# Optimization experiments

Hardware: AMD Instinct MI355X
Metric: run time of the kernel (lower is better)

The kernel has to match this reference:

```python
import math
import jax, jax.numpy as jnp
import numpy as np

NUM_HEADS = 32
NUM_KV_HEADS = 8
HEAD_SIZE = 128
FEATURE_DIM = 64
SEQ_LEN = 2048
WINDOW_SIZE = 64
EPS = 1e-12
MASK_VALUE = -100000000.0


def _make_masks(n: int, w: int):
    # block-diagonal ones(w,w) tiles, plus the rolled (sub-diagonal) tiles
    m = math.ceil(n / w)
    mask = np.kron(np.eye(m), np.ones((w, w)))
    mask = mask + np.roll(mask, -w, axis=-1)
    mask = mask[:n, :n]
    mask_window = np.tril(mask).astype(bool)[None, None]          # [1,1,n,n]
    mask_linear = np.tril(1.0 - mask).astype(bool)[None, None]    # [1,1,n,n]
    return jnp.asarray(mask_window), jnp.asarray(mask_linear)


def _feature_map(w, x):
    # f(x) = clamp(cat(softmax(xW), softmax(-xW)), min=eps)
    z = jnp.einsum('hdf,bhld->bhlf', w, x)
    return jnp.clip(
        jnp.concatenate([jax.nn.softmax(z, axis=-1), jax.nn.softmax(-z, axis=-1)], axis=-1),
        EPS, None)


def setup_inputs() -> dict:
    key = jax.random.key(0)
    ks = jax.random.split(key, 6)
    return {
        'query': jax.random.normal(ks[0], (SEQ_LEN, NUM_HEADS * HEAD_SIZE), dtype=jnp.float32),
        'key': jax.random.normal(ks[1], (SEQ_LEN, NUM_KV_HEADS * HEAD_SIZE), dtype=jnp.float32),
        'value': jax.random.normal(ks[2], (SEQ_LEN, NUM_KV_HEADS * HEAD_SIZE), dtype=jnp.float32),
        'fmap_q_w': 0.02 * jax.random.normal(ks[3], (NUM_HEADS, HEAD_SIZE, FEATURE_DIM), dtype=jnp.float32),
        'fmap_k_w': 0.02 * jax.random.normal(ks[4], (NUM_HEADS, HEAD_SIZE, FEATURE_DIM), dtype=jnp.float32),
        'window_factors': jax.random.normal(ks[5], (1, NUM_HEADS, 1, 1), dtype=jnp.float32),
    }


def reference(query, key, value, fmap_q_w, fmap_k_w, window_factors):
    T = query.shape[0]
    q = query.reshape(T, NUM_HEADS, HEAD_SIZE)
    k = key.reshape(T, NUM_KV_HEADS, HEAD_SIZE)
    v = value.reshape(T, NUM_KV_HEADS, HEAD_SIZE)
    rep = NUM_HEADS // NUM_KV_HEADS
    k = jnp.repeat(k, rep, axis=1)
    v = jnp.repeat(v, rep, axis=1)
    # [T,H,D] -> [1,H,T,D]
    q = jnp.moveaxis(q, 0, -2)[None]
    k = jnp.moveaxis(k, 0, -2)[None]
    v = jnp.moveaxis(v, 0, -2)[None]

    f_q = _feature_map(fmap_q_w, q)  # [1,H,T,2F]
    f_k = _feature_map(fmap_k_w, k)
    wf = jax.nn.sigmoid(window_factors)

    mask_window, mask_linear = _make_masks(SEQ_LEN, WINDOW_SIZE)
    mask_window = mask_window[:, :, :T, :T]
    mask_linear = mask_linear[:, :, :T, :T]

    # sliding-window softmax term
    a_sm = jnp.einsum('bhmd,bhnd->bhmn', q, k) * (HEAD_SIZE ** -0.5)
    a_sm = jnp.where(mask_window, a_sm, MASK_VALUE)
    a_sm_max = jnp.max(a_sm, axis=-1, keepdims=True)
    a_sm = wf * jnp.exp(a_sm - a_sm_max)
    sum_sm = jnp.sum(a_sm, axis=-1, keepdims=True)

    # linear feature-map term (linear_factor = 1)
    a_ln = jnp.einsum('bhmd,bhnd->bhmn', f_q, f_k)
    a_ln = jnp.where(mask_linear, a_ln, 0.0)
    sum_ln = jnp.sum(a_ln, axis=-1, keepdims=True)

    y = jnp.einsum('bhmn,bhnd->bhmd', a_sm + a_ln, v)
    return y / (sum_sm + sum_ln)
```

## Files before the change

### kernel.cpp

```cpp
#include <hip/hip_runtime.h>
#include <math.h>

#define T_SEQ 2048
#define NH    32
#define NKV   8
#define HS    128
#define FD    64
#define NBLK  32
#define SCAN_NB 30
#define EPSF  1e-12f
#define LDP   136
#define STP   129

typedef unsigned short u16;
typedef __bf16 bf16x8 __attribute__((ext_vector_type(8)));
typedef float  f32x4  __attribute__((ext_vector_type(4)));

__device__ __forceinline__ u16 f2b(float f) {
  unsigned u = __builtin_bit_cast(unsigned, f);
  return (u16)((u + 0x7fffu + ((u >> 16) & 1u)) >> 16);
}

#define FKT_OFF 0
#define ST_OFF  16777216
#define VT_OFF  54525952
#define WT_OFF  58720256
#define KB_OFF  59768832

__device__ __forceinline__ void stage_bf(u16* buf, const u16* __restrict__ src, int tid) {
#pragma unroll
  for (int i = 0; i < 4; ++i) {
    int idx = tid * 8 + i * 2048, rr = idx >> 7, c = idx & 127;
    *(uint4*)(buf + rr * LDP + c) = *(const uint4*)(src + idx);
  }
}
__device__ __forceinline__ void stage_vt(u16* buf, const u16* __restrict__ vts,
                                         int rofs, int kb0, int B, int tid) {
#pragma unroll
  for (int i = 0; i < 4; ++i) {
    int idx = tid * 8 + i * 2048, rr = idx >> 7, c = idx & 127;
    int key = (c < 64) ? (kb0 * 64 + c) : (B * 64 + (c - 64));
    *(uint4*)(buf + rr * LDP + c) = *(const uint4*)(vts + (size_t)(rr + rofs) * T_SEQ + key);
  }
}

__global__ __launch_bounds__(256) void k_pre(
    const float* __restrict__ wq, const float* __restrict__ wk,
    const float* __restrict__ vg,
    u16* __restrict__ WT, u16* __restrict__ VT)
{
  __shared__ float sB[128 * 68];
  const int bx = blockIdx.x, tid = threadIdx.x;

  if (bx < 64) {
    const int h = bx >> 1, isk = bx & 1;
    const float* src = (isk ? wk : wq) + (size_t)h * HS * FD;
    for (int idx = tid * 4; idx < 8192; idx += 1024) {
      int r = idx >> 6, c = idx & 63;
      *(float4*)(sB + r * 68 + c) = *(const float4*)(src + idx);
    }
    __syncthreads();
    u16* dst = WT + ((size_t)(isk * NH + h)) * 8192;
    for (int i = 0; i < 8; ++i) {
      int ch = tid + i * 256;
      int f = ch >> 5, d4 = (ch & 31) * 4;
      ushort4 u;
      u.x = f2b(sB[(d4 + 0) * 68 + f]);
      u.y = f2b(sB[(d4 + 1) * 68 + f]);
      u.z = f2b(sB[(d4 + 2) * 68 + f]);
      u.w = f2b(sB[(d4 + 3) * 68 + f]);
      *(ushort4*)(dst + f * 128 + d4) = u;
    }
  } else {
    const int idx2 = bx - 64;
    const int b = idx2 & 31, kvh = idx2 >> 5;
    float* sV = sB;
    for (int idx = tid * 4; idx < 8192; idx += 1024) {
      int r = idx >> 7, c = idx & 127;
      *(float4*)(sV + r * 129 + c) = *(const float4*)(vg + (size_t)(b * 64 + r) * (NKV * HS) + kvh * HS + c);
    }
    __syncthreads();
    const int lane = tid & 63, w = tid >> 6;
#pragma unroll
    for (int i = 0; i < 32; ++i) {
      int d = w * 32 + i;
      VT[((size_t)(kvh * 128 + d)) * T_SEQ + b * 64 + lane] = f2b(sV[lane * 129 + d]);
    }
  }
}

__global__ __launch_bounds__(256) void k_fmap(
    const float* __restrict__ kg, const u16* __restrict__ WT,
    u16* __restrict__ FKT, u16* __restrict__ KBB)
{
  __shared__ __align__(16) u16 smem[2 * 64 * 136];
  u16* sX = smem;
  u16* sW = smem + 64 * 136;
  const int lt = blockIdx.x, h = blockIdx.y;
  const int tid = threadIdx.x, lane = tid & 63, w = tid >> 6;
  const int quad = lane >> 4, txn = lane & 15;

  const float* xbase = kg + (h >> 2) * HS;
  const int    xstr  = NKV * HS;
  for (int idx = tid * 4; idx < 8192; idx += 1024) {
    int r = idx >> 7, c = idx & 127;
    float4 v4 = *(const float4*)(xbase + (size_t)(lt * 64 + r) * xstr + c);
    ushort4 u; u.x = f2b(v4.x); u.y = f2b(v4.y); u.z = f2b(v4.z); u.w = f2b(v4.w);
    *(ushort4*)(sX + r * 136 + c) = u;
  }
  const u16* wt = WT + ((size_t)(NH + h)) * 8192;
  for (int i = 0; i < 4; ++i) {
    int ch = tid + i * 256;
    int row = ch >> 4, d8 = (ch & 15) * 8;
    *(uint4*)(sW + row * 136 + d8) = *(const uint4*)(wt + row * 128 + d8);
  }
  __syncthreads();

  if ((h & 3) == 0) {
    u16* ob = KBB + ((size_t)((h >> 2) * NBLK + lt)) * 8192;
    for (int i = 0; i < 4; ++i) {
      int ch = tid + i * 256;
      int row = ch >> 4, d8 = (ch & 15) * 8;
      *(uint4*)(ob + row * 128 + d8) = *(const uint4*)(sX + row * 136 + d8);
    }
  }

  const int arow = w * 16 + txn;
  const f32x4 vzero = {0.f, 0.f, 0.f, 0.f};
  f32x4 zt[4] = {vzero, vzero, vzero, vzero};
#pragma unroll
  for (int ks = 0; ks < 4; ++ks) {
    bf16x8 a = *(const bf16x8*)(sX + arow * 136 + ks * 32 + quad * 8);
#pragma unroll
    for (int nt = 0; nt < 4; ++nt) {
      bf16x8 bb = *(const bf16x8*)(sW + (nt * 16 + txn) * 136 + ks * 32 + quad * 8);
      zt[nt] = __builtin_amdgcn_mfma_f32_16x16x32_bf16(a, bb, zt[nt], 0, 0, 0);
    }
  }

  float E1[4][4], E2[4][4];
#pragma unroll
  for (int r = 0; r < 4; ++r) {
    float zv[4];
    float mx = -1e30f, mn = 1e30f;
#pragma unroll
    for (int nt = 0; nt < 4; ++nt) {
      zv[nt] = zt[nt][r];
      mx = fmaxf(mx, zv[nt]); mn = fminf(mn, zv[nt]);
    }
#pragma unroll
    for (int o = 1; o < 16; o <<= 1) {
      mx = fmaxf(mx, __shfl_xor(mx, o));
      mn = fminf(mn, __shfl_xor(mn, o));
    }
    float e1[4], e2[4], s1 = 0.f, s2 = 0.f;
#pragma unroll
    for (int nt = 0; nt < 4; ++nt) {
      e1[nt] = __expf(zv[nt] - mx); s1 += e1[nt];
      e2[nt] = __expf(mn - zv[nt]); s2 += e2[nt];
    }
#pragma unroll
    for (int o = 1; o < 16; o <<= 1) { s1 += __shfl_xor(s1, o); s2 += __shfl_xor(s2, o); }
    float r1 = 1.f / s1, r2 = 1.f / s2;
#pragma unroll
    for (int nt = 0; nt < 4; ++nt) {
      E1[r][nt] = fmaxf(e1[nt] * r1, EPSF);
      E2[r][nt] = fmaxf(e2[nt] * r2, EPSF);
    }
  }

  __syncthreads();

#pragma unroll
  for (int r = 0; r < 4; ++r) {
    int j = w * 16 + quad * 4 + r;
#pragma unroll
    for (int nt = 0; nt < 4; ++nt) {
      sX[(nt * 16 + txn) * 68 + j]        = f2b(E1[r][nt]);
      sX[(nt * 16 + txn + 64) * 68 + j]   = f2b(E2[r][nt]);
    }
  }
  __syncthreads();
  u16* ob = FKT + (size_t)h * 128 * T_SEQ + lt * 64;
  for (int i = 0; i < 8; ++i) {
    int ch = tid + i * 256;
    int row = ch >> 4, j4 = (ch & 15) * 4;
    *(ushort4*)(ob + (size_t)row * T_SEQ + j4) = *(const ushort4*)(sX + row * 68 + j4);
  }
}

__global__ __launch_bounds__(256) void k_scan(
    const u16* __restrict__ FKT, const u16* __restrict__ VT, u16* __restrict__ ST)
{
  __shared__ __align__(16) u16 sVT[16 * 72];
  __shared__ __align__(16) u16 sFK[64 * 72];
  const int L = blockIdx.x + 8 * blockIdx.y + 16 * blockIdx.z;
  const int xcd = L & 7, j = L >> 3;
  const int hsub = j & 3, fh = (j >> 2) & 1, dc = j >> 3;
  const int h = xcd * 4 + hsub;
  const int tid = threadIdx.x, lane = tid & 63, w = tid >> 6;
  const int quad = lane >> 4, txn = lane & 15;
  const bool doz = (dc == 0);

  bf16x8 vone;
#pragma unroll
  for (int jj = 0; jj < 8; ++jj) vone[jj] = (__bf16)1.0f;

  const u16* vbase = VT + ((size_t)((h >> 2) * 128 + dc * 16)) * T_SEQ;
  const u16* fbase = FKT + ((size_t)(h * 128 + fh * 64)) * T_SEQ;

  const int srow = tid >> 4, sj4 = (tid & 15) * 4;
  ushort4 rv, rf[4];
  rv = *(const ushort4*)(vbase + (size_t)srow * T_SEQ + sj4);
#pragma unroll
  for (int i = 0; i < 4; ++i) {
    int ch = tid + i * 256;
    int fr = ch >> 4, fj4 = (ch & 15) * 4;
    rf[i] = *(const ushort4*)(fbase + (size_t)fr * T_SEQ + fj4);
  }

  const f32x4 vzero = {0.f, 0.f, 0.f, 0.f};
  f32x4 acc = vzero, zacc = vzero;

  for (int b = 0; b < SCAN_NB; ++b) {
    __syncthreads();
    *(ushort4*)(sVT + srow * 72 + sj4) = rv;
#pragma unroll
    for (int i = 0; i < 4; ++i) {
      int ch = tid + i * 256;
      int fr = ch >> 4, fj4 = (ch & 15) * 4;
      *(ushort4*)(sFK + fr * 72 + fj4) = rf[i];
    }
    __syncthreads();
    if (b + 1 < SCAN_NB) {
      rv = *(const ushort4*)(vbase + (size_t)srow * T_SEQ + (b + 1) * 64 + sj4);
#pragma unroll
      for (int i = 0; i < 4; ++i) {
        int ch = tid + i * 256;
        int fr = ch >> 4, fj4 = (ch & 15) * 4;
        rf[i] = *(const ushort4*)(fbase + (size_t)fr * T_SEQ + (b + 1) * 64 + fj4);
      }
    }
#pragma unroll
    for (int ks = 0; ks < 2; ++ks) {
      bf16x8 a  = *(const bf16x8*)(sVT + txn * 72 + ks * 32 + quad * 8);
      bf16x8 bb = *(const bf16x8*)(sFK + (w * 16 + txn) * 72 + ks * 32 + quad * 8);
      acc = __builtin_amdgcn_mfma_f32_16x16x32_bf16(a, bb, acc, 0, 0, 0);
      if (doz) zacc = __builtin_amdgcn_mfma_f32_16x16x32_bf16(vone, bb, zacc, 0, 0, 0);
    }
    u16* Sb = ST + (((size_t)(h * NBLK + b)) * STP + dc * 16) * 128 + fh * 64;
#pragma unroll
    for (int r = 0; r < 4; ++r)
      Sb[(quad * 4 + r) * 128 + w * 16 + txn] = f2b(acc[r]);
    if (doz && quad == 0)
      ST[(((size_t)(h * NBLK + b)) * STP + 128) * 128 + fh * 64 + w * 16 + txn] = f2b(zacc[0]);
  }
}

__global__ __launch_bounds__(256, 4) void k_main(
    const float* __restrict__ qg, const u16* __restrict__ KBB,
    const u16* __restrict__ WT, const u16* __restrict__ ST,
    const u16* __restrict__ VT, const float* __restrict__ wfac,
    float* __restrict__ out)
{
  __shared__ __align__(16) u16 RA[64 * LDP];
  __shared__ __align__(16) u16 RB[64 * LDP];
  __shared__ __align__(16) u16 sz[128];
  const int L = blockIdx.x + 32 * blockIdx.y;
  const int xcd = L & 7, j = L >> 3;
  const int hsub = j & 3, B = j >> 2;
  const int h = xcd * 4 + hsub;
  const int tid = threadIdx.x;
  const int lane = tid & 63, w = tid >> 6;
  const int quad = lane >> 4, txn = lane & 15;
  const int arow = w * 16 + txn;
  const int koff = quad * 8;

  const f32x4 vzero = {0.f, 0.f, 0.f, 0.f};
  f32x4 y[8];
#pragma unroll
  for (int t = 0; t < 8; ++t) y[t] = vzero;
  float sln[4] = {0.f, 0.f, 0.f, 0.f};
  const bf16x8 bzero = {0, 0, 0, 0, 0, 0, 0, 0};

  const int kb0 = (B >= 1) ? B - 1 : 0;
  const u16* ktB   = KBB + ((size_t)((h >> 2) * NBLK + B)) * 8192;
  const u16* ktP   = KBB + ((size_t)((h >> 2) * NBLK + kb0)) * 8192;
  const u16* vts   = VT  + (size_t)((h >> 2) * 128) * T_SEQ;

  for (int idx = tid * 4; idx < 8192; idx += 1024) {
    int r = idx >> 7, c = idx & 127;
    float4 v4 = *(const float4*)(qg + (size_t)(B * 64 + r) * (NH * HS) + h * HS + c);
    ushort4 u; u.x = f2b(v4.x); u.y = f2b(v4.y); u.z = f2b(v4.z); u.w = f2b(v4.w);
    *(ushort4*)(RA + r * LDP + c) = u;
  }
  if (B >= 2) stage_bf(RB, WT + (size_t)h * 8192, tid);
  __syncthreads();

  f32x4 zt[4] = {vzero, vzero, vzero, vzero};
  if (B >= 2) {
#pragma unroll
    for (int ks = 0; ks < 4; ++ks) {
      bf16x8 a = *(const bf16x8*)(RA + arow * LDP + ks * 32 + koff);
#pragma unroll
      for (int nt = 0; nt < 4; ++nt) {
        bf16x8 bb = *(const bf16x8*)(RB + (nt * 16 + txn) * LDP + ks * 32 + koff);
        zt[nt] = __builtin_amdgcn_mfma_f32_16x16x32_bf16(a, bb, zt[nt], 0, 0, 0);
      }
    }
  }
  __syncthreads();
  stage_bf(RB, ktB, tid);

  unsigned Epk[4][4];
  if (B >= 2) {
#pragma unroll
    for (int r = 0; r < 4; ++r) {
      float zv[4];
      float mx = -1e30f, mn = 1e30f;
#pragma unroll
      for (int nt = 0; nt < 4; ++nt) {
        zv[nt] = zt[nt][r];
        mx = fmaxf(mx, zv[nt]); mn = fminf(mn, zv[nt]);
      }
#pragma unroll
      for (int o = 1; o < 16; o <<= 1) {
        mx = fmaxf(mx, __shfl_xor(mx, o));
        mn = fminf(mn, __shfl_xor(mn, o));
      }
      float e1[4], e2[4], s1 = 0.f, s2 = 0.f;
#pragma unroll
      for (int nt = 0; nt < 4; ++nt) {
        e1[nt] = __expf(zv[nt] - mx); s1 += e1[nt];
        e2[nt] = __expf(mn - zv[nt]); s2 += e2[nt];
      }
#pragma unroll
      for (int o = 1; o < 16; o <<= 1) { s1 += __shfl_xor(s1, o); s2 += __shfl_xor(s2, o); }
      float r1 = 1.f / s1, r2 = 1.f / s2;
#pragma unroll
      for (int nt = 0; nt < 4; ++nt) {
        unsigned lo = f2b(fmaxf(e1[nt] * r1, EPSF));
        unsigned hi = f2b(fmaxf(e2[nt] * r2, EPSF));
        Epk[r][nt] = lo | (hi << 16);
      }
    }
  }
  __syncthreads();

  f32x4 s[8];
#pragma unroll
  for (int t = 0; t < 8; ++t) s[t] = vzero;
#pragma unroll
  for (int ks = 0; ks < 4; ++ks) {
    bf16x8 a = *(const bf16x8*)(RA + arow * LDP + ks * 32 + koff);
#pragma unroll
    for (int t = 0; t < 4; ++t) {
      bf16x8 bb = *(const bf16x8*)(RB + (t * 16 + txn) * LDP + ks * 32 + koff);
      s[4 + t] = __builtin_amdgcn_mfma_f32_16x16x32_bf16(a, bb, s[4 + t], 0, 0, 0);
    }
  }

  if (B >= 1) {
    __syncthreads();
    stage_bf(RB, ktP, tid);
    __syncthreads();
#pragma unroll
    for (int ks = 0; ks < 4; ++ks) {
      bf16x8 a = *(const bf16x8*)(RA + arow * LDP + ks * 32 + koff);
#pragma unroll
      for (int t = 0; t < 4; ++t) {
        bf16x8 bb = *(const bf16x8*)(RB + (t * 16 + txn) * LDP + ks * 32 + koff);
        s[t] = __builtin_amdgcn_mfma_f32_16x16x32_bf16(a, bb, s[t], 0, 0, 0);
      }
    }
  }

  float wf = wfac[h];
  wf = 1.f / (1.f + __expf(-wf));
  const float scale = 0.08838834764831845f;
  float ssum[4];
#pragma unroll
  for (int r = 0; r < 4; ++r) {
    const int irow = w * 16 + quad * 4 + r;
    float sv[8];
    float m = -1e30f;
#pragma unroll
    for (int t = 0; t < 8; ++t) {
      float x = s[t][r] * scale;
      bool msk = (t < 4) ? (B == 0) : ((t - 4) * 16 + txn > irow);
      x = msk ? -1e30f : x;
      sv[t] = x;
      m = fmaxf(m, x);
    }
#pragma unroll
    for (int o = 1; o < 16; o <<= 1) m = fmaxf(m, __shfl_xor(m, o));
    float ss = 0.f;
#pragma unroll
    for (int t = 0; t < 8; ++t) {
      float e = (sv[t] > -1e29f) ? wf * __expf(sv[t] - m) : 0.f;
      ss += e;
      RA[irow * LDP + t * 16 + txn] = f2b(e);
    }
#pragma unroll
    for (int o = 1; o < 16; o <<= 1) ss += __shfl_xor(ss, o);
    ssum[r] = ss;
  }
  __syncthreads();

  stage_vt(RB, vts, 0, kb0, B, tid);
  __syncthreads();
#pragma unroll
  for (int ks = 0; ks < 4; ++ks) {
    if (B == 0 && ks < 2) continue;
    bf16x8 a = *(const bf16x8*)(RA + arow * LDP + ks * 32 + koff);
#pragma unroll
    for (int t = 0; t < 4; ++t) {
      bf16x8 bb = *(const bf16x8*)(RB + (t * 16 + txn) * LDP + ks * 32 + koff);
      y[t] = __builtin_amdgcn_mfma_f32_16x16x32_bf16(a, bb, y[t], 0, 0, 0);
    }
  }
  __syncthreads();

  stage_vt(RB, vts, 64, kb0, B, tid);
  __syncthreads();
#pragma unroll
  for (int ks = 0; ks < 4; ++ks) {
    if (B == 0 && ks < 2) continue;
    bf16x8 a = *(const bf16x8*)(RA + arow * LDP + ks * 32 + koff);
#pragma unroll
    for (int t = 4; t < 8; ++t) {
      bf16x8 bb = *(const bf16x8*)(RB + (t * 16 + txn - 64) * LDP + ks * 32 + koff);
      y[t] = __builtin_amdgcn_mfma_f32_16x16x32_bf16(a, bb, y[t], 0, 0, 0);
    }
  }

  if (B >= 2) {
    __syncthreads();
#pragma unroll
    for (int r = 0; r < 4; ++r) {
      int row = w * 16 + quad * 4 + r;
#pragma unroll
      for (int nt = 0; nt < 4; ++nt) {
        RA[row * LDP + nt * 16 + txn]      = (u16)(Epk[r][nt] & 0xffffu);
        RA[row * LDP + 64 + nt * 16 + txn] = (u16)(Epk[r][nt] >> 16);
      }
    }
    const u16* ssrc = ST + ((size_t)(h * NBLK + (B - 2))) * (STP * 128);
    stage_bf(RB, ssrc, tid);
    if (tid < 32) *(ushort4*)(sz + tid * 4) = *(const ushort4*)(ssrc + 16384 + tid * 4);
    __syncthreads();
    f32x4 yz = vzero;
#pragma unroll
    for (int ks = 0; ks < 4; ++ks) {
      bf16x8 a = *(const bf16x8*)(RA + arow * LDP + ks * 32 + koff);
#pragma unroll
      for (int t = 0; t < 4; ++t) {
        bf16x8 bb = *(const bf16x8*)(RB + (t * 16 + txn) * LDP + ks * 32 + koff);
        y[t] = __builtin_amdgcn_mfma_f32_16x16x32_bf16(a, bb, y[t], 0, 0, 0);
      }
      bf16x8 bz = (txn == 0) ? *(const bf16x8*)(sz + ks * 32 + koff) : bzero;
      yz = __builtin_amdgcn_mfma_f32_16x16x32_bf16(a, bz, yz, 0, 0, 0);
    }
    __syncthreads();
    stage_bf(RB, ssrc + 8192, tid);
    __syncthreads();
#pragma unroll
    for (int ks = 0; ks < 4; ++ks) {
      bf16x8 a = *(const bf16x8*)(RA + arow * LDP + ks * 32 + koff);
#pragma unroll
      for (int t = 4; t < 8; ++t) {
        bf16x8 bb = *(const bf16x8*)(RB + (t * 16 + txn - 64) * LDP + ks * 32 + koff);
        y[t] = __builtin_amdgcn_mfma_f32_16x16x32_bf16(a, bb, y[t], 0, 0, 0);
      }
    }
#pragma unroll
    for (int r = 0; r < 4; ++r) sln[r] = __shfl(yz[r], lane & 48);
  }

  const size_t obase = ((size_t)h * T_SEQ + B * 64) * HS;
#pragma unroll
  for (int r = 0; r < 4; ++r) {
    float inv = 1.f / (ssum[r] + sln[r]);
    int irow = w * 16 + quad * 4 + r;
#pragma unroll
    for (int t = 0; t < 8; ++t)
      out[obase + (size_t)irow * HS + t * 16 + txn] = y[t][r] * inv;
  }
}

extern "C" void kernel_launch(void* const* d_in, const int* in_sizes, int n_in,
                              void* d_out, int out_size, void* d_ws, size_t ws_size,
                              hipStream_t stream) {
  const float* q    = (const float*)d_in[0];
  const float* k    = (const float*)d_in[1];
  const float* v    = (const float*)d_in[2];
  const float* wq   = (const float*)d_in[3];
  const float* wk   = (const float*)d_in[4];
  const float* wfac = (const float*)d_in[5];
  float* out = (float*)d_out;
  char* wsb = (char*)d_ws;

  u16* FKT = (u16*)(wsb + FKT_OFF);
  u16* ST  = (u16*)(wsb + ST_OFF);
  u16* VT  = (u16*)(wsb + VT_OFF);
  u16* WT  = (u16*)(wsb + WT_OFF);
  u16* KBB = (u16*)(wsb + KB_OFF);

  k_pre  <<<dim3(320),      256, 0, stream>>>(wq, wk, v, WT, VT);
  k_fmap <<<dim3(NBLK, NH), 256, 0, stream>>>(k, WT, FKT, KBB);
  k_scan <<<dim3(8, 2, NH), 256, 0, stream>>>(FKT, VT, ST);
  k_main <<<dim3(NBLK, NH), 256, 0, stream>>>(q, KBB, WT, ST, VT, wfac, out);
}
```

Baseline: 161.5 us.

## Split k_main key and output columns across two wave groups with 512 threads

The main attention kernel moves from 256 to 512 threads per block. The new waves split the key columns of the score tile and the output columns of the PV and state products, with each wave group doing half the MFMA work. Row max and row sums are now combined across the two wave halves through a small shared-memory buffer with extra barriers. Staging is reorganised into half-tiles so each group works from the right rows. The aim is more waves in flight to hide latency, at the cost of extra synchronisation and redundant feature-map projection work in both halves.

```diff
diff --git a/kernel.cpp b/kernel.cpp
--- a/kernel.cpp
+++ b/kernel.cpp
@@ -26,23 +26,6 @@
 #define VT_OFF  54525952
 #define WT_OFF  58720256
 #define KB_OFF  59768832
-
-__device__ __forceinline__ void stage_bf(u16* buf, const u16* __restrict__ src, int tid) {
-#pragma unroll
-  for (int i = 0; i < 4; ++i) {
-    int idx = tid * 8 + i * 2048, rr = idx >> 7, c = idx & 127;
-    *(uint4*)(buf + rr * LDP + c) = *(const uint4*)(src + idx);
-  }
-}
-__device__ __forceinline__ void stage_vt(u16* buf, const u16* __restrict__ vts,
-                                         int rofs, int kb0, int B, int tid) {
-#pragma unroll
-  for (int i = 0; i < 4; ++i) {
-    int idx = tid * 8 + i * 2048, rr = idx >> 7, c = idx & 127;
-    int key = (c < 64) ? (kb0 * 64 + c) : (B * 64 + (c - 64));
-    *(uint4*)(buf + rr * LDP + c) = *(const uint4*)(vts + (size_t)(rr + rofs) * T_SEQ + key);
-  }
-}
 
 __global__ __launch_bounds__(256) void k_pre(
     const float* __restrict__ wq, const float* __restrict__ wk,
@@ -257,7 +240,7 @@
   }
 }
 
-__global__ __launch_bounds__(256, 4) void k_main(
+__global__ __launch_bounds__(512, 6) void k_main(
     const float* __restrict__ qg, const u16* __restrict__ KBB,
     const u16* __restrict__ WT, const u16* __restrict__ ST,
     const u16* __restrict__ VT, const float* __restrict__ wfac,
@@ -266,35 +249,75 @@
   __shared__ __align__(16) u16 RA[64 * LDP];
   __shared__ __align__(16) u16 RB[64 * LDP];
   __shared__ __align__(16) u16 sz[128];
+  __shared__ float sred[256];
   const int L = blockIdx.x + 32 * blockIdx.y;
-  const int xcd = L & 7, j = L >> 3;
-  const int hsub = j & 3, B = j >> 2;
+  const int xcd = L & 7, jj = L >> 3;
+  const int hsub = jj & 3, B = jj >> 2;
   const int h = xcd * 4 + hsub;
   const int tid = threadIdx.x;
   const int lane = tid & 63, w = tid >> 6;
+  const int wq_ = w & 3, wt = w >> 2;
   const int quad = lane >> 4, txn = lane & 15;
-  const int arow = w * 16 + txn;
+  const int arow = wq_ * 16 + txn;
   const int koff = quad * 8;
 
   const f32x4 vzero = {0.f, 0.f, 0.f, 0.f};
-  f32x4 y[8];
-#pragma unroll
-  for (int t = 0; t < 8; ++t) y[t] = vzero;
+  f32x4 y[4];
+#pragma unroll
+  for (int t = 0; t < 4; ++t) y[t] = vzero;
   float sln[4] = {0.f, 0.f, 0.f, 0.f};
   const bf16x8 bzero = {0, 0, 0, 0, 0, 0, 0, 0};
 
   const int kb0 = (B >= 1) ? B - 1 : 0;
-  const u16* ktB   = KBB + ((size_t)((h >> 2) * NBLK + B)) * 8192;
-  const u16* ktP   = KBB + ((size_t)((h >> 2) * NBLK + kb0)) * 8192;
-  const u16* vts   = VT  + (size_t)((h >> 2) * 128) * T_SEQ;
-
-  for (int idx = tid * 4; idx < 8192; idx += 1024) {
+  const u16* ktB = KBB + ((size_t)((h >> 2) * NBLK + B)) * 8192;
+  const u16* ktP = KBB + ((size_t)((h >> 2) * NBLK + kb0)) * 8192;
+  const u16* vts = VT  + (size_t)((h >> 2) * 128) * T_SEQ;
+  const u16* wqt = WT  + (size_t)h * 8192;
+  const u16* ssrc = ST + ((size_t)(h * NBLK + (B >= 2 ? B - 2 : 0))) * (STP * 128);
+
+  auto stage_full = [&](const u16* __restrict__ src) {
+#pragma unroll
+    for (int i = 0; i < 2; ++i) {
+      int idx = tid * 8 + i * 4096, rr = idx >> 7, c = idx & 127;
+      *(uint4*)(RB + rr * LDP + c) = *(const uint4*)(src + idx);
+    }
+  };
+  auto stage_qk = [&](int p) {
+#pragma unroll
+    for (int i = 0; i < 2; ++i) {
+      int idx = tid * 8 + i * 4096, rr = idx >> 7, c = idx & 127;
+      const u16* src = (rr < 32) ? (ktB + (p * 32 + rr) * 128)
+                                 : (ktP + (p * 32 + rr - 32) * 128);
+      *(uint4*)(RB + rr * LDP + c) = *(const uint4*)(src + c);
+    }
+  };
+  auto stage_v = [&](int p) {
+#pragma unroll
+    for (int i = 0; i < 2; ++i) {
+      int idx = tid * 8 + i * 4096, rr = idx >> 7, c = idx & 127;
+      int d = (rr < 32) ? (p * 32 + rr) : (64 + p * 32 + rr - 32);
+      int key = (c < 64) ? (kb0 * 64 + c) : (B * 64 + (c - 64));
+      *(uint4*)(RB + rr * LDP + c) = *(const uint4*)(vts + (size_t)d * T_SEQ + key);
+    }
+  };
+  auto stage_s = [&](int p) {
+#pragma unroll
+    for (int i = 0; i < 2; ++i) {
+      int idx = tid * 8 + i * 4096, rr = idx >> 7, c = idx & 127;
+      int d = (rr < 32) ? (p * 32 + rr) : (64 + p * 32 + rr - 32);
+      *(uint4*)(RB + rr * LDP + c) = *(const uint4*)(ssrc + d * 128 + c);
+    }
+  };
+
+#pragma unroll
+  for (int i = 0; i < 4; ++i) {
+    int idx = tid * 4 + i * 2048;
     int r = idx >> 7, c = idx & 127;
     float4 v4 = *(const float4*)(qg + (size_t)(B * 64 + r) * (NH * HS) + h * HS + c);
     ushort4 u; u.x = f2b(v4.x); u.y = f2b(v4.y); u.z = f2b(v4.z); u.w = f2b(v4.w);
     *(ushort4*)(RA + r * LDP + c) = u;
   }
-  if (B >= 2) stage_bf(RB, WT + (size_t)h * 8192, tid);
+  if (B >= 2) stage_full(wqt);
   __syncthreads();
 
   f32x4 zt[4] = {vzero, vzero, vzero, vzero};
@@ -310,7 +333,7 @@
     }
   }
   __syncthreads();
-  stage_bf(RB, ktB, tid);
+  stage_qk(0);
 
   unsigned Epk[4][4];
   if (B >= 2) {
@@ -347,130 +370,156 @@
   }
   __syncthreads();
 
-  f32x4 s[8];
-#pragma unroll
-  for (int t = 0; t < 8; ++t) s[t] = vzero;
+  f32x4 s[4];
+#pragma unroll
+  for (int t = 0; t < 4; ++t) s[t] = vzero;
 #pragma unroll
   for (int ks = 0; ks < 4; ++ks) {
     bf16x8 a = *(const bf16x8*)(RA + arow * LDP + ks * 32 + koff);
 #pragma unroll
-    for (int t = 0; t < 4; ++t) {
-      bf16x8 bb = *(const bf16x8*)(RB + (t * 16 + txn) * LDP + ks * 32 + koff);
-      s[4 + t] = __builtin_amdgcn_mfma_f32_16x16x32_bf16(a, bb, s[4 + t], 0, 0, 0);
-    }
-  }
-
-  if (B >= 1) {
-    __syncthreads();
-    stage_bf(RB, ktP, tid);
-    __syncthreads();
-#pragma unroll
-    for (int ks = 0; ks < 4; ++ks) {
-      bf16x8 a = *(const bf16x8*)(RA + arow * LDP + ks * 32 + koff);
-#pragma unroll
-      for (int t = 0; t < 4; ++t) {
-        bf16x8 bb = *(const bf16x8*)(RB + (t * 16 + txn) * LDP + ks * 32 + koff);
-        s[t] = __builtin_amdgcn_mfma_f32_16x16x32_bf16(a, bb, s[t], 0, 0, 0);
-      }
+    for (int tl = 0; tl < 2; ++tl) {
+      if (wt == 0 && B == 0) continue;
+      int row = (wt ? 0 : 32) + tl * 16 + txn;
+      bf16x8 bb = *(const bf16x8*)(RB + row * LDP + ks * 32 + koff);
+      s[tl] = __builtin_amdgcn_mfma_f32_16x16x32_bf16(a, bb, s[tl], 0, 0, 0);
+    }
+  }
+  __syncthreads();
+  stage_qk(1);
+  __syncthreads();
+#pragma unroll
+  for (int ks = 0; ks < 4; ++ks) {
+    bf16x8 a = *(const bf16x8*)(RA + arow * LDP + ks * 32 + koff);
+#pragma unroll
+    for (int tl = 0; tl < 2; ++tl) {
+      if (wt == 0 && B == 0) continue;
+      int row = (wt ? 0 : 32) + tl * 16 + txn;
+      bf16x8 bb = *(const bf16x8*)(RB + row * LDP + ks * 32 + koff);
+      s[2 + tl] = __builtin_amdgcn_mfma_f32_16x16x32_bf16(a, bb, s[2 + tl], 0, 0, 0);
     }
   }
 
   float wf = wfac[h];
   wf = 1.f / (1.f + __expf(-wf));
   const float scale = 0.08838834764831845f;
+  float mh[4];
+#pragma unroll
+  for (int r = 0; r < 4; ++r) {
+    const int irow = wq_ * 16 + quad * 4 + r;
+    float m = -1e30f;
+#pragma unroll
+    for (int sl = 0; sl < 4; ++sl) {
+      float x = s[sl][r] * scale;
+      bool msk = wt ? (sl * 16 + txn > irow) : (B == 0);
+      x = msk ? -1e30f : x;
+      s[sl][r] = x;
+      m = fmaxf(m, x);
+    }
+#pragma unroll
+    for (int o = 1; o < 16; o <<= 1) m = fmaxf(m, __shfl_xor(m, o));
+    mh[r] = m;
+  }
+  if (txn == 0) {
+#pragma unroll
+    for (int r = 0; r < 4; ++r) sred[wt * 64 + wq_ * 16 + quad * 4 + r] = mh[r];
+  }
+  __syncthreads();
+
   float ssum[4];
 #pragma unroll
   for (int r = 0; r < 4; ++r) {
-    const int irow = w * 16 + quad * 4 + r;
-    float sv[8];
-    float m = -1e30f;
-#pragma unroll
-    for (int t = 0; t < 8; ++t) {
-      float x = s[t][r] * scale;
-      bool msk = (t < 4) ? (B == 0) : ((t - 4) * 16 + txn > irow);
-      x = msk ? -1e30f : x;
-      sv[t] = x;
-      m = fmaxf(m, x);
-    }
-#pragma unroll
-    for (int o = 1; o < 16; o <<= 1) m = fmaxf(m, __shfl_xor(m, o));
+    const int irow = wq_ * 16 + quad * 4 + r;
+    float m = fmaxf(mh[r], sred[(wt ^ 1) * 64 + wq_ * 16 + quad * 4 + r]);
     float ss = 0.f;
 #pragma unroll
-    for (int t = 0; t < 8; ++t) {
-      float e = (sv[t] > -1e29f) ? wf * __expf(sv[t] - m) : 0.f;
+    for (int sl = 0; sl < 4; ++sl) {
+      float e = (s[sl][r] > -1e29f) ? wf * __expf(s[sl][r] - m) : 0.f;
       ss += e;
-      RA[irow * LDP + t * 16 + txn] = f2b(e);
+      RA[irow * LDP + wt * 64 + sl * 16 + txn] = f2b(e);
     }
 #pragma unroll
     for (int o = 1; o < 16; o <<= 1) ss += __shfl_xor(ss, o);
     ssum[r] = ss;
   }
-  __syncthreads();
-
-  stage_vt(RB, vts, 0, kb0, B, tid);
-  __syncthreads();
+  if (txn == 0) {
+#pragma unroll
+    for (int r = 0; r < 4; ++r) sred[128 + wt * 64 + wq_ * 16 + quad * 4 + r] = ssum[r];
+  }
+  stage_v(0);
+  __syncthreads();
+#pragma unroll
+  for (int r = 0; r < 4; ++r)
+    ssum[r] += sred[128 + (wt ^ 1) * 64 + wq_ * 16 + quad * 4 + r];
+
 #pragma unroll
   for (int ks = 0; ks < 4; ++ks) {
     if (B == 0 && ks < 2) continue;
     bf16x8 a = *(const bf16x8*)(RA + arow * LDP + ks * 32 + koff);
 #pragma unroll
-    for (int t = 0; t < 4; ++t) {
-      bf16x8 bb = *(const bf16x8*)(RB + (t * 16 + txn) * LDP + ks * 32 + koff);
-      y[t] = __builtin_amdgcn_mfma_f32_16x16x32_bf16(a, bb, y[t], 0, 0, 0);
-    }
-  }
-  __syncthreads();
-
-  stage_vt(RB, vts, 64, kb0, B, tid);
+    for (int tl = 0; tl < 2; ++tl) {
+      int row = wt * 32 + tl * 16 + txn;
+      bf16x8 bb = *(const bf16x8*)(RB + row * LDP + ks * 32 + koff);
+      y[tl] = __builtin_amdgcn_mfma_f32_16x16x32_bf16(a, bb, y[tl], 0, 0, 0);
+    }
+  }
+  __syncthreads();
+  stage_v(1);
   __syncthreads();
 #pragma unroll
   for (int ks = 0; ks < 4; ++ks) {
     if (B == 0 && ks < 2) continue;
     bf16x8 a = *(const bf16x8*)(RA + arow * LDP + ks * 32 + koff);
 #pragma unroll
-    for (int t = 4; t < 8; ++t) {
-      bf16x8 bb = *(const bf16x8*)(RB + (t * 16 + txn - 64) * LDP + ks * 32 + koff);
-      y[t] = __builtin_amdgcn_mfma_f32_16x16x32_bf16(a, bb, y[t], 0, 0, 0);
-    }
-  }
+    for (int tl = 0; tl < 2; ++tl) {
+      int row = wt * 32 + tl * 16 + txn;
+      bf16x8 bb = *(const bf16x8*)(RB + row * LDP + ks * 32 + koff);
+      y[2 + tl] = __builtin_amdgcn_mfma_f32_16x16x32_bf16(a, bb, y[2 + tl], 0, 0, 0);
+    }
+  }
+  __syncthreads();
 
   if (B >= 2) {
-    __syncthreads();
 #pragma unroll
     for (int r = 0; r < 4; ++r) {
-      int row = w * 16 + quad * 4 + r;
+      int row = wq_ * 16 + quad * 4 + r;
 #pragma unroll
       for (int nt = 0; nt < 4; ++nt) {
-        RA[row * LDP + nt * 16 + txn]      = (u16)(Epk[r][nt] & 0xffffu);
-        RA[row * LDP + 64 + nt * 16 + txn] = (u16)(Epk[r][nt] >> 16);
-      }
-    }
-    const u16* ssrc = ST + ((size_t)(h * NBLK + (B - 2))) * (STP * 128);
-    stage_bf(RB, ssrc, tid);
-    if (tid < 32) *(ushort4*)(sz + tid * 4) = *(const ushort4*)(ssrc + 16384 + tid * 4);
-    __syncthreads();
-    f32x4 yz = vzero;
+        u16 val = wt ? (u16)(Epk[r][nt] >> 16) : (u16)(Epk[r][nt] & 0xffffu);
+        RA[row * LDP + wt * 64 + nt * 16 + txn] = val;
+      }
+    }
+  }
+  stage_s(0);
+  if (tid < 32) *(ushort4*)(sz + tid * 4) = *(const ushort4*)(ssrc + 16384 + tid * 4);
+  __syncthreads();
+
+  f32x4 yz = vzero;
+  if (B >= 2) {
 #pragma unroll
     for (int ks = 0; ks < 4; ++ks) {
       bf16x8 a = *(const bf16x8*)(RA + arow * LDP + ks * 32 + koff);
 #pragma unroll
-      for (int t = 0; t < 4; ++t) {
-        bf16x8 bb = *(const bf16x8*)(RB + (t * 16 + txn) * LDP + ks * 32 + koff);
-        y[t] = __builtin_amdgcn_mfma_f32_16x16x32_bf16(a, bb, y[t], 0, 0, 0);
+      for (int tl = 0; tl < 2; ++tl) {
+        int row = wt * 32 + tl * 16 + txn;
+        bf16x8 bb = *(const bf16x8*)(RB + row * LDP + ks * 32 + koff);
+        y[tl] = __builtin_amdgcn_mfma_f32_16x16x32_bf16(a, bb, y[tl], 0, 0, 0);
       }
       bf16x8 bz = (txn == 0) ? *(const bf16x8*)(sz + ks * 32 + koff) : bzero;
       yz = __builtin_amdgcn_mfma_f32_16x16x32_bf16(a, bz, yz, 0, 0, 0);
     }
-    __syncthreads();
-    stage_bf(RB, ssrc + 8192, tid);
-    __syncthreads();
+  }
+  __syncthreads();
+  stage_s(1);
+  __syncthreads();
+  if (B >= 2) {
 #pragma unroll
     for (int ks = 0; ks < 4; ++ks) {
       bf16x8 a = *(const bf16x8*)(RA + arow * LDP + ks * 32 + koff);
 #pragma unroll
-      for (int t = 4; t < 8; ++t) {
-        bf16x8 bb = *(const bf16x8*)(RB + (t * 16 + txn - 64) * LDP + ks * 32 + koff);
-        y[t] = __builtin_amdgcn_mfma_f32_16x16x32_bf16(a, bb, y[t], 0, 0, 0);
+      for (int tl = 0; tl < 2; ++tl) {
+        int row = wt * 32 + tl * 16 + txn;
+        bf16x8 bb = *(const bf16x8*)(RB + row * LDP + ks * 32 + koff);
+        y[2 + tl] = __builtin_amdgcn_mfma_f32_16x16x32_bf16(a, bb, y[2 + tl], 0, 0, 0);
       }
     }
 #pragma unroll
@@ -481,10 +530,12 @@
 #pragma unroll
   for (int r = 0; r < 4; ++r) {
     float inv = 1.f / (ssum[r] + sln[r]);
-    int irow = w * 16 + quad * 4 + r;
-#pragma unroll
-    for (int t = 0; t < 8; ++t)
-      out[obase + (size_t)irow * HS + t * 16 + txn] = y[t][r] * inv;
+    int irow = wq_ * 16 + quad * 4 + r;
+#pragma unroll
+    for (int yl = 0; yl < 4; ++yl) {
+      int t = wt * 4 + yl;
+      out[obase + (size_t)irow * HS + t * 16 + txn] = y[yl][r] * inv;
+    }
   }
 }
 
@@ -509,5 +560,5 @@
   k_pre  <<<dim3(320),      256, 0, stream>>>(wq, wk, v, WT, VT);
   k_fmap <<<dim3(NBLK, NH), 256, 0, stream>>>(k, WT, FKT, KBB);
   k_scan <<<dim3(8, 2, NH), 256, 0, stream>>>(FKT, VT, ST);
-  k_main <<<dim3(NBLK, NH), 256, 0, stream>>>(q, KBB, WT, ST, VT, wfac, out);
+  k_main <<<dim3(NBLK, NH), 512, 0, stream>>>(q, KBB, WT, ST, VT, wfac, out);
 }
```

After: 163.2 us. Within noise of the previous version (+1.0%).

## Fuse prep and key feature-map kernels, block FKT layout, double-buffer scan

Applied to the files above, without the earlier changes.

Merges the weight/V transpose kernel and the key feature-map kernel into a single launch, with the fmap blocks reading and transposing the fp32 key weights directly instead of going through WT. FKT is stored in contiguous per-block tiles so the scan reads it with unit stride, and the scan kernel double-buffers its shared tiles to drop one barrier per iteration. In the main kernel, the query-weight MFMA operands are read straight from global memory instead of staged in LDS, which removes a barrier and lets K staging overlap with that matmul. This saves one kernel launch and some synchronisation, at the cost of uncoalesced global operand loads and a heavier mixed-role prep grid.

```diff
diff --git a/kernel.cpp b/kernel.cpp
--- a/kernel.cpp
+++ b/kernel.cpp
@@ -44,23 +44,26 @@
   }
 }
 
-__global__ __launch_bounds__(256) void k_pre(
+__global__ __launch_bounds__(256) void k_prep(
     const float* __restrict__ wq, const float* __restrict__ wk,
-    const float* __restrict__ vg,
-    u16* __restrict__ WT, u16* __restrict__ VT)
+    const float* __restrict__ vg, const float* __restrict__ kg,
+    u16* __restrict__ WT, u16* __restrict__ VT,
+    u16* __restrict__ FKT, u16* __restrict__ KBB)
 {
-  __shared__ float sB[128 * 68];
+  __shared__ __align__(16) u16 smem[2 * 64 * 136];
   const int bx = blockIdx.x, tid = threadIdx.x;
-
-  if (bx < 64) {
-    const int h = bx >> 1, isk = bx & 1;
-    const float* src = (isk ? wk : wq) + (size_t)h * HS * FD;
+  const int lane = tid & 63, w = tid >> 6;
+  const int quad = lane >> 4, txn = lane & 15;
+
+  if (bx < 32) {
+    float* sB = (float*)smem;
+    const float* src = wq + (size_t)bx * HS * FD;
     for (int idx = tid * 4; idx < 8192; idx += 1024) {
       int r = idx >> 6, c = idx & 63;
       *(float4*)(sB + r * 68 + c) = *(const float4*)(src + idx);
     }
     __syncthreads();
-    u16* dst = WT + ((size_t)(isk * NH + h)) * 8192;
+    u16* dst = WT + (size_t)bx * 8192;
     for (int i = 0; i < 8; ++i) {
       int ch = tid + i * 256;
       int f = ch >> 5, d4 = (ch & 31) * 4;
@@ -71,34 +74,30 @@
       u.w = f2b(sB[(d4 + 3) * 68 + f]);
       *(ushort4*)(dst + f * 128 + d4) = u;
     }
-  } else {
-    const int idx2 = bx - 64;
+    return;
+  }
+
+  if (bx < 288) {
+    const int idx2 = bx - 32;
     const int b = idx2 & 31, kvh = idx2 >> 5;
-    float* sV = sB;
+    float* sV = (float*)smem;
     for (int idx = tid * 4; idx < 8192; idx += 1024) {
       int r = idx >> 7, c = idx & 127;
       *(float4*)(sV + r * 129 + c) = *(const float4*)(vg + (size_t)(b * 64 + r) * (NKV * HS) + kvh * HS + c);
     }
     __syncthreads();
-    const int lane = tid & 63, w = tid >> 6;
 #pragma unroll
     for (int i = 0; i < 32; ++i) {
       int d = w * 32 + i;
       VT[((size_t)(kvh * 128 + d)) * T_SEQ + b * 64 + lane] = f2b(sV[lane * 129 + d]);
     }
-  }
-}
-
-__global__ __launch_bounds__(256) void k_fmap(
-    const float* __restrict__ kg, const u16* __restrict__ WT,
-    u16* __restrict__ FKT, u16* __restrict__ KBB)
-{
-  __shared__ __align__(16) u16 smem[2 * 64 * 136];
+    return;
+  }
+
+  const int j2 = bx - 288;
+  const int lt = j2 & 31, h = j2 >> 5;
   u16* sX = smem;
   u16* sW = smem + 64 * 136;
-  const int lt = blockIdx.x, h = blockIdx.y;
-  const int tid = threadIdx.x, lane = tid & 63, w = tid >> 6;
-  const int quad = lane >> 4, txn = lane & 15;
 
   const float* xbase = kg + (h >> 2) * HS;
   const int    xstr  = NKV * HS;
@@ -108,11 +107,17 @@
     ushort4 u; u.x = f2b(v4.x); u.y = f2b(v4.y); u.z = f2b(v4.z); u.w = f2b(v4.w);
     *(ushort4*)(sX + r * 136 + c) = u;
   }
-  const u16* wt = WT + ((size_t)(NH + h)) * 8192;
-  for (int i = 0; i < 4; ++i) {
-    int ch = tid + i * 256;
-    int row = ch >> 4, d8 = (ch & 15) * 8;
-    *(uint4*)(sW + row * 136 + d8) = *(const uint4*)(wt + row * 128 + d8);
+  {
+    const float* wsrc = wk + (size_t)h * (HS * FD);
+    const int d = tid >> 1, f0 = (tid & 1) * 32;
+#pragma unroll
+    for (int i = 0; i < 8; ++i) {
+      float4 v4 = *(const float4*)(wsrc + d * 64 + f0 + i * 4);
+      sW[(f0 + i * 4 + 0) * 136 + d] = f2b(v4.x);
+      sW[(f0 + i * 4 + 1) * 136 + d] = f2b(v4.y);
+      sW[(f0 + i * 4 + 2) * 136 + d] = f2b(v4.z);
+      sW[(f0 + i * 4 + 3) * 136 + d] = f2b(v4.w);
+    }
   }
   __syncthreads();
 
@@ -181,19 +186,19 @@
     }
   }
   __syncthreads();
-  u16* ob = FKT + (size_t)h * 128 * T_SEQ + lt * 64;
+  u16* ob = FKT + ((size_t)(h * 32 + lt)) * 8192;
   for (int i = 0; i < 8; ++i) {
     int ch = tid + i * 256;
     int row = ch >> 4, j4 = (ch & 15) * 4;
-    *(ushort4*)(ob + (size_t)row * T_SEQ + j4) = *(const ushort4*)(sX + row * 68 + j4);
+    *(ushort4*)(ob + row * 64 + j4) = *(const ushort4*)(sX + row * 68 + j4);
   }
 }
 
 __global__ __launch_bounds__(256) void k_scan(
     const u16* __restrict__ FKT, const u16* __restrict__ VT, u16* __restrict__ ST)
 {
-  __shared__ __align__(16) u16 sVT[16 * 72];
-  __shared__ __align__(16) u16 sFK[64 * 72];
+  __shared__ __align__(16) u16 sVT[2][16 * 72];
+  __shared__ __align__(16) u16 sFK[2][64 * 72];
   const int L = blockIdx.x + 8 * blockIdx.y + 16 * blockIdx.z;
   const int xcd = L & 7, j = L >> 3;
   const int hsub = j & 3, fh = (j >> 2) & 1, dc = j >> 3;
@@ -207,7 +212,7 @@
   for (int jj = 0; jj < 8; ++jj) vone[jj] = (__bf16)1.0f;
 
   const u16* vbase = VT + ((size_t)((h >> 2) * 128 + dc * 16)) * T_SEQ;
-  const u16* fbase = FKT + ((size_t)(h * 128 + fh * 64)) * T_SEQ;
+  const u16* fbase = FKT + (size_t)(h * 32) * 8192 + fh * 4096;
 
   const int srow = tid >> 4, sj4 = (tid & 15) * 4;
   ushort4 rv, rf[4];
@@ -216,20 +221,22 @@
   for (int i = 0; i < 4; ++i) {
     int ch = tid + i * 256;
     int fr = ch >> 4, fj4 = (ch & 15) * 4;
-    rf[i] = *(const ushort4*)(fbase + (size_t)fr * T_SEQ + fj4);
+    rf[i] = *(const ushort4*)(fbase + fr * 64 + fj4);
   }
 
   const f32x4 vzero = {0.f, 0.f, 0.f, 0.f};
   f32x4 acc = vzero, zacc = vzero;
+  int cur = 0;
 
   for (int b = 0; b < SCAN_NB; ++b) {
-    __syncthreads();
-    *(ushort4*)(sVT + srow * 72 + sj4) = rv;
+    u16* dV = sVT[cur];
+    u16* dF = sFK[cur];
+    *(ushort4*)(dV + srow * 72 + sj4) = rv;
 #pragma unroll
     for (int i = 0; i < 4; ++i) {
       int ch = tid + i * 256;
       int fr = ch >> 4, fj4 = (ch & 15) * 4;
-      *(ushort4*)(sFK + fr * 72 + fj4) = rf[i];
+      *(ushort4*)(dF + fr * 72 + fj4) = rf[i];
     }
     __syncthreads();
     if (b + 1 < SCAN_NB) {
@@ -238,13 +245,13 @@
       for (int i = 0; i < 4; ++i) {
         int ch = tid + i * 256;
         int fr = ch >> 4, fj4 = (ch & 15) * 4;
-        rf[i] = *(const ushort4*)(fbase + (size_t)fr * T_SEQ + (b + 1) * 64 + fj4);
+        rf[i] = *(const ushort4*)(fbase + (size_t)(b + 1) * 8192 + fr * 64 + fj4);
       }
     }
 #pragma unroll
     for (int ks = 0; ks < 2; ++ks) {
-      bf16x8 a  = *(const bf16x8*)(sVT + txn * 72 + ks * 32 + quad * 8);
-      bf16x8 bb = *(const bf16x8*)(sFK + (w * 16 + txn) * 72 + ks * 32 + quad * 8);
+      bf16x8 a  = *(const bf16x8*)(dV + txn * 72 + ks * 32 + quad * 8);
+      bf16x8 bb = *(const bf16x8*)(dF + (w * 16 + txn) * 72 + ks * 32 + quad * 8);
       acc = __builtin_amdgcn_mfma_f32_16x16x32_bf16(a, bb, acc, 0, 0, 0);
       if (doz) zacc = __builtin_amdgcn_mfma_f32_16x16x32_bf16(vone, bb, zacc, 0, 0, 0);
     }
@@ -254,6 +261,7 @@
       Sb[(quad * 4 + r) * 128 + w * 16 + txn] = f2b(acc[r]);
     if (doz && quad == 0)
       ST[(((size_t)(h * NBLK + b)) * STP + 128) * 128 + fh * 64 + w * 16 + txn] = f2b(zacc[0]);
+    cur ^= 1;
   }
 }
 
@@ -267,8 +275,8 @@
   __shared__ __align__(16) u16 RB[64 * LDP];
   __shared__ __align__(16) u16 sz[128];
   const int L = blockIdx.x + 32 * blockIdx.y;
-  const int xcd = L & 7, j = L >> 3;
-  const int hsub = j & 3, B = j >> 2;
+  const int xcd = L & 7, jj = L >> 3;
+  const int hsub = jj & 3, B = jj >> 2;
   const int h = xcd * 4 + hsub;
   const int tid = threadIdx.x;
   const int lane = tid & 63, w = tid >> 6;
@@ -284,18 +292,24 @@
   const bf16x8 bzero = {0, 0, 0, 0, 0, 0, 0, 0};
 
   const int kb0 = (B >= 1) ? B - 1 : 0;
-  const u16* ktB   = KBB + ((size_t)((h >> 2) * NBLK + B)) * 8192;
-  const u16* ktP   = KBB + ((size_t)((h >> 2) * NBLK + kb0)) * 8192;
-  const u16* vts   = VT  + (size_t)((h >> 2) * 128) * T_SEQ;
-
-  for (int idx = tid * 4; idx < 8192; idx += 1024) {
-    int r = idx >> 7, c = idx & 127;
-    float4 v4 = *(const float4*)(qg + (size_t)(B * 64 + r) * (NH * HS) + h * HS + c);
-    ushort4 u; u.x = f2b(v4.x); u.y = f2b(v4.y); u.z = f2b(v4.z); u.w = f2b(v4.w);
-    *(ushort4*)(RA + r * LDP + c) = u;
-  }
-  if (B >= 2) stage_bf(RB, WT + (size_t)h * 8192, tid);
-  __syncthreads();
+  const u16* ktB = KBB + ((size_t)((h >> 2) * NBLK + B)) * 8192;
+  const u16* ktP = KBB + ((size_t)((h >> 2) * NBLK + kb0)) * 8192;
+  const u16* vts = VT  + (size_t)((h >> 2) * 128) * T_SEQ;
+  const u16* wqt = WT  + (size_t)h * 8192;
+  const u16* ssrc = ST + ((size_t)(h * NBLK + (B >= 2 ? B - 2 : 0))) * (STP * 128);
+
+  {
+    const float* qb = qg + (size_t)(B * 64 + w * 16) * (NH * HS) + h * HS;
+#pragma unroll
+    for (int i = 0; i < 8; ++i) {
+      int idx = lane + i * 64;
+      int r = idx >> 5, c4 = (idx & 31) * 4;
+      float4 v4 = *(const float4*)(qb + (size_t)r * (NH * HS) + c4);
+      ushort4 u; u.x = f2b(v4.x); u.y = f2b(v4.y); u.z = f2b(v4.z); u.w = f2b(v4.w);
+      *(ushort4*)(RA + (w * 16 + r) * LDP + c4) = u;
+    }
+  }
+  stage_bf(RB, ktB, tid);
 
   f32x4 zt[4] = {vzero, vzero, vzero, vzero};
   if (B >= 2) {
@@ -304,13 +318,11 @@
       bf16x8 a = *(const bf16x8*)(RA + arow * LDP + ks * 32 + koff);
 #pragma unroll
       for (int nt = 0; nt < 4; ++nt) {
-        bf16x8 bb = *(const bf16x8*)(RB + (nt * 16 + txn) * LDP + ks * 32 + koff);
+        bf16x8 bb = *(const bf16x8*)(wqt + (nt * 16 + txn) * 128 + ks * 32 + koff);
         zt[nt] = __builtin_amdgcn_mfma_f32_16x16x32_bf16(a, bb, zt[nt], 0, 0, 0);
       }
     }
   }
-  __syncthreads();
-  stage_bf(RB, ktB, tid);
 
   unsigned Epk[4][4];
   if (B >= 2) {
@@ -445,7 +457,6 @@
         RA[row * LDP + 64 + nt * 16 + txn] = (u16)(Epk[r][nt] >> 16);
       }
     }
-    const u16* ssrc = ST + ((size_t)(h * NBLK + (B - 2))) * (STP * 128);
     stage_bf(RB, ssrc, tid);
     if (tid < 32) *(ushort4*)(sz + tid * 4) = *(const ushort4*)(ssrc + 16384 + tid * 4);
     __syncthreads();
@@ -506,8 +517,7 @@
   u16* WT  = (u16*)(wsb + WT_OFF);
   u16* KBB = (u16*)(wsb + KB_OFF);
 
-  k_pre  <<<dim3(320),      256, 0, stream>>>(wq, wk, v, WT, VT);
-  k_fmap <<<dim3(NBLK, NH), 256, 0, stream>>>(k, WT, FKT, KBB);
+  k_prep <<<dim3(1312),     256, 0, stream>>>(wq, wk, v, k, WT, VT, FKT, KBB);
   k_scan <<<dim3(8, 2, NH), 256, 0, stream>>>(FKT, VT, ST);
   k_main <<<dim3(NBLK, NH), 256, 0, stream>>>(q, KBB, WT, ST, VT, wfac, out);
 }
```

Measured after the change: 160.3 us. About the same (-0.8%).
